# Optimization experiments

Measured on AMD Instinct MI355X. Metric: run time of the kernel, lower is better.

## Reference

```python
import jax, jax.numpy as jnp
import numpy as np

NUM_HEAD = 8   # in_channels // 64 for in_channels=512
DIM = 8        # per-head dim (== num_head in this module)
H_CH = NUM_HEAD * DIM  # 64
SCALE = DIM ** (-0.5)


def _conv(x, w, b, padding):
    # x: [N,C,H,W], w: [O,I,kh,kw]
    out = jax.lax.conv_general_dilated(
        x, w, window_strides=(1, 1), padding=padding,
        dimension_numbers=("NCHW", "OIHW", "NCHW"))
    return out + b[None, :, None, None]


def setup_inputs() -> dict:
    key = jax.random.key(0)
    ks = jax.random.split(key, 4)
    N, C, H, W = 4, 512, 48, 48
    x = jax.random.normal(ks[0], (N, C, H, W), dtype=jnp.float32)
    qkv_w = jax.random.normal(ks[1], (3 * H_CH, C, 1, 1), dtype=jnp.float32) * 0.05
    qkv_b = jnp.zeros((3 * H_CH,), dtype=jnp.float32)
    pos_w = jax.random.normal(ks[2], (H_CH, H_CH, 3, 3), dtype=jnp.float32) * 0.05
    pos_b = jnp.zeros((H_CH,), dtype=jnp.float32)
    res_w = jax.random.normal(ks[3], (C, H_CH, 1, 1), dtype=jnp.float32) * 0.05
    res_b = jnp.zeros((C,), dtype=jnp.float32)
    return {"x": x, "qkv_w": qkv_w, "qkv_b": qkv_b,
            "pos_w": pos_w, "pos_b": pos_b,
            "res_w": res_w, "res_b": res_b}


def reference(x, qkv_w, qkv_b, pos_w, pos_b, res_w, res_b):
    N, C, H, W = x.shape
    L = H * W
    # 1x1 conv QKV projection -> [N, 3h, H, W]
    qkv = _conv(x, qkv_w, qkv_b, "VALID")
    # [N, num_head, 3*dim, L]
    qkv = qkv.reshape(N, NUM_HEAD, 3 * DIM, L)
    q, k, v = qkv[:, :, :DIM], qkv[:, :, DIM:2 * DIM], qkv[:, :, 2 * DIM:]
    # attn = q^T @ k * scale : [N, nh, L, L], softmax over keys (last dim)
    attn = jnp.einsum("nhdq,nhdk->nhqk", q, k) * SCALE
    attn = jax.nn.softmax(attn, axis=-1)
    # out = v @ attn^T : [N, nh, dim, L]
    out = jnp.einsum("nhdk,nhqk->nhdq", v, attn)
    out = out.reshape(N, H_CH, H, W)
    # positional branch: 3x3 conv on v
    pos = _conv(v.reshape(N, H_CH, H, W), pos_w, pos_b, "SAME")
    out = out + pos
    # resume 1x1 conv -> [N, out_channels, H, W]
    return _conv(out, res_w, res_b, "VALID")
```

## Files before the change

### kernel.cpp

```cpp
#include <hip/hip_runtime.h>

#define L_ATT 2304
#define QSCALE_LOG2E 0.5100695712f

using bh8 = __attribute__((ext_vector_type(8))) short;
using f4  = __attribute__((ext_vector_type(4))) float;

#if __has_builtin(__builtin_amdgcn_exp2f)
#define EXP2(x) __builtin_amdgcn_exp2f(x)
#else
#define EXP2(x) exp2f(x)
#endif

__device__ inline short f2b(float f) {
    union { float f; unsigned u; } c; c.f = f;
    unsigned r = (c.u + 0x7FFFu + ((c.u >> 16) & 1u)) >> 16;
    return (short)r;
}
__device__ inline float b2f(short s) {
    union { unsigned u; float f; } c;
    c.u = ((unsigned)(unsigned short)s) << 16;
    return c.f;
}
__device__ inline int packhi(float lo, float hi) {
    return (int)__builtin_amdgcn_perm(__float_as_uint(hi), __float_as_uint(lo), 0x07060302u);
}

__global__ __launch_bounds__(256) void prep_kernel(
    const float* __restrict__ x, const float* __restrict__ qkv_w,
    const float* __restrict__ res_w, const float* __restrict__ pos_w,
    short* __restrict__ xt, short* __restrict__ wqb,
    short* __restrict__ reswb, short* __restrict__ wqp)
{
    __shared__ float s[64][68];
    const int g = blockIdx.x;
    if (g < 272) {
        int j = g * 256 + threadIdx.x;
        if (j < 24576) {
            float4 v = ((const float4*)qkv_w)[j];
            short4 o = { f2b(v.x), f2b(v.y), f2b(v.z), f2b(v.w) };
            *(short4*)(wqb + (size_t)j * 4) = o;
        } else if (j < 32768) {
            int idx = j - 24576;
            float4 v = ((const float4*)res_w)[idx];
            short4 o = { f2b(v.x), f2b(v.y), f2b(v.z), f2b(v.w) };
            *(short4*)(reswb + (size_t)idx * 4) = o;
        } else {
            int e = j - 32768;
            wqp[e] = f2b(pos_w[(size_t)(e & 4095) * 9 + (e >> 12)]);
        }
        return;
    }
    const int gg = g - 272;
    const int l0 = (gg % 36) * 64, k0 = ((gg / 36) & 7) * 64, n = gg / 288;
    const int tr = threadIdx.x >> 4, tc4 = (threadIdx.x & 15) * 4;
    const float* xp = x + ((size_t)n * 512 + k0) * L_ATT + l0;
#pragma unroll
    for (int r = 0; r < 4; ++r)
        *(float4*)&s[tr + r * 16][tc4] =
            *(const float4*)(xp + (size_t)(tr + r * 16) * L_ATT + tc4);
    __syncthreads();
    short* op = xt + ((size_t)n * L_ATT + l0) * 512 + k0;
#pragma unroll
    for (int r = 0; r < 4; ++r) {
        int l = tr + r * 16;
        short4 o = { f2b(s[tc4 + 0][l]), f2b(s[tc4 + 1][l]),
                     f2b(s[tc4 + 2][l]), f2b(s[tc4 + 3][l]) };
        *(short4*)(op + (size_t)l * 512 + tc4) = o;
    }
}

__global__ __launch_bounds__(256) void qkv_kernel(
    const short* __restrict__ xt, const short* __restrict__ wqb,
    const float* __restrict__ qkv_b, short* __restrict__ qt8,
    short* __restrict__ kt8, short* __restrict__ vt, short* __restrict__ vle)
{
    const int g = blockIdx.x;
    const int xcd = g & 7, rr = g >> 3;
    const int y = rr % 3, grp = rr / 3;
    const int code = grp * 8 + xcd;
    const int l0 = (code % 72) * 32, oc0 = y * 64, n = code / 72;

    const int lane = threadIdx.x & 63, wave = threadIdx.x >> 6;
    const int col = lane & 15, quad = lane >> 4;
    const int ocb = oc0 + wave * 16;

    f4 acc[2];
    acc[0] = (f4){0.f, 0.f, 0.f, 0.f};
    acc[1] = (f4){0.f, 0.f, 0.f, 0.f};

    const short* arow = wqb + (size_t)(ocb + col) * 512 + quad * 8;
    const short* brow = xt + ((size_t)n * L_ATT + l0 + col) * 512 + quad * 8;

#pragma unroll 4
    for (int k0 = 0; k0 < 512; k0 += 32) {
        bh8 af = *(const bh8*)(arow + k0);
        bh8 b0 = *(const bh8*)(brow + k0);
        bh8 b1 = *(const bh8*)(brow + (size_t)16 * 512 + k0);
        acc[0] = __builtin_amdgcn_mfma_f32_16x16x32_bf16(af, b0, acc[0], 0, 0, 0);
        acc[1] = __builtin_amdgcn_mfma_f32_16x16x32_bf16(af, b1, acc[1], 0, 0, 0);
    }

    const int obase = ocb + quad * 4;
    const int h = obase / 24;
    const int r0 = obase - h * 24;
    const int slice = n * 8 + h;

#pragma unroll
    for (int nt = 0; nt < 2; ++nt) {
        int l = l0 + nt * 16 + col;
        float v[4];
#pragma unroll
        for (int reg = 0; reg < 4; ++reg) v[reg] = acc[nt][reg] + qkv_b[obase + reg];
        if (r0 < 8) {
            short4 o = { f2b(v[0] * QSCALE_LOG2E), f2b(v[1] * QSCALE_LOG2E),
                         f2b(v[2] * QSCALE_LOG2E), f2b(v[3] * QSCALE_LOG2E) };
            *(short4*)(qt8 + ((size_t)slice * L_ATT + l) * 8 + r0) = o;
        } else if (r0 < 16) {
            short4 o = { f2b(v[0]), f2b(v[1]), f2b(v[2]), f2b(v[3]) };
            *(short4*)(kt8 + ((size_t)slice * L_ATT + l) * 8 + (r0 - 8)) = o;
        } else {
            short4 o = { f2b(v[0]), f2b(v[1]), f2b(v[2]), f2b(v[3]) };
            int d0 = r0 - 16;
#pragma unroll
            for (int reg = 0; reg < 4; ++reg)
                vt[((size_t)slice * 8 + d0 + reg) * L_ATT + l] = ((short*)&o)[reg];
            *(short4*)(vle + ((size_t)n * L_ATT + l) * 64 + h * 8 + d0) = o;
        }
    }
}

__global__ __launch_bounds__(256) void attnpos_kernel(
    const short* __restrict__ qt8, const short* __restrict__ kt8,
    const short* __restrict__ vt, const short* __restrict__ vle,
    const short* __restrict__ wqp, const float* __restrict__ pbias,
    float* __restrict__ pnum, float* __restrict__ pls, short* __restrict__ pcv)
{
    __shared__ short smem[2064];
    const int g = blockIdx.x;
    const int tid = threadIdx.x;
    const int lane = tid & 63, wave = tid >> 6;
    const int col = lane & 15, quad = lane >> 4;

    if (g < 1152) {
        const int h = g & 7, r = g >> 3;
        const int n = r / 36;
        const int rem = r - n * 36;
        const int qt = rem >> 1, half = rem & 1;
        const int q0 = qt * 128;
        const int kbase = half * 1152;
        const int slice = n * 8 + h;

        const short* qs  = qt8 + (size_t)slice * L_ATT * 8;
        const short* ks8 = kt8 + (size_t)slice * L_ATT * 8;
        const short* vb  = vt  + (size_t)slice * 8 * L_ATT;

        if (tid < 16) smem[2048 + tid] = (tid < 8) ? (short)0x3F80 : (short)0;

        bh8 zero8 = {0, 0, 0, 0, 0, 0, 0, 0};
        bh8 qf[2];
#pragma unroll
        for (int f = 0; f < 2; ++f) {
            qf[f] = zero8;
            if (quad == 0)
                qf[f] = *(const bh8*)(qs + (size_t)(q0 + wave * 32 + f * 16 + col) * 8);
        }

        const int kxor = (quad == 0) ? 512 : 0;
        int kidx[4];
#pragma unroll
        for (int nt = 0; nt < 4; ++nt)
            kidx[nt] = (quad == 0) ? (nt * 16 + col) * 8 : 2056;
        const int vxor = (col < 8) ? 512 : 0;
        int vidx[2];
#pragma unroll
        for (int ks = 0; ks < 2; ++ks)
            vidx[ks] = (col < 8)
                     ? 1024 + col * 64 + ((ks * 32 + quad * 8 + col * 8) & 63)
                     : ((col == 8) ? 2048 : 2056);

        const int ksl = ((lane >> 5) & 1) * 32 + ((lane >> 2) & 1) * 16
                      + ((lane >> 3) & 3) * 4 + (lane & 3);
        const int vd = lane >> 3, vkc = (lane & 7) * 8;
        const int vsl = 1024 + vd * 64 + ((vkc + vd * 8) & 63);

        if (wave == 0)
            *(uint4*)&smem[ksl * 8] = *(const uint4*)(ks8 + (size_t)(kbase + lane) * 8);
        else if (wave == 1)
            *(uint4*)&smem[vsl] = *(const uint4*)(vb + (size_t)vd * L_ATT + kbase + vkc);
        __syncthreads();

        f4 oacc[2];
        oacc[0] = (f4){0.f, 0.f, 0.f, 0.f};
        oacc[1] = (f4){0.f, 0.f, 0.f, 0.f};

        int sofs = 512;
        for (int t = 0; t < 18; ++t) {
            const int par = (t + 1) & 1;
            uint4 dk, dv;
            if (wave == par * 2)
                dk = *(const uint4*)(ks8 + (size_t)(kbase + (t + 1) * 64 + lane) * 8);
            else if (wave == par * 2 + 1)
                dv = *(const uint4*)(vb + (size_t)vd * L_ATT + kbase + (t + 1) * 64 + vkc);

            bh8 kf[4], vf[2];
#pragma unroll
            for (int nt = 0; nt < 4; ++nt) kf[nt] = *(const bh8*)&smem[kidx[nt]];
#pragma unroll
            for (int ks = 0; ks < 2; ++ks) vf[ks] = *(const bh8*)&smem[vidx[ks]];

            __builtin_amdgcn_s_setprio(1);
#pragma unroll
            for (int f = 0; f < 2; ++f) {
                f4 s[4];
#pragma unroll
                for (int nt = 0; nt < 4; ++nt) {
                    f4 z = (f4){0.f, 0.f, 0.f, 0.f};
                    s[nt] = __builtin_amdgcn_mfma_f32_16x16x32_bf16(kf[nt], qf[f], z, 0, 0, 0);
                }
                float e[4][4];
#pragma unroll
                for (int nt = 0; nt < 4; ++nt)
#pragma unroll
                    for (int reg = 0; reg < 4; ++reg)
                        e[nt][reg] = EXP2(s[nt][reg]);
#pragma unroll
                for (int ks = 0; ks < 2; ++ks) {
                    union { int i[4]; bh8 v; } pu;
                    pu.i[0] = packhi(e[2 * ks][0],     e[2 * ks][1]);
                    pu.i[1] = packhi(e[2 * ks][2],     e[2 * ks][3]);
                    pu.i[2] = packhi(e[2 * ks + 1][0], e[2 * ks + 1][1]);
                    pu.i[3] = packhi(e[2 * ks + 1][2], e[2 * ks + 1][3]);
                    oacc[f] = __builtin_amdgcn_mfma_f32_16x16x32_bf16(vf[ks], pu.v, oacc[f], 0, 0, 0);
                }
            }
            __builtin_amdgcn_s_setprio(0);

            if (wave == par * 2)          *(uint4*)&smem[sofs + ksl * 8] = dk;
            else if (wave == par * 2 + 1) *(uint4*)&smem[sofs + vsl] = dv;

#pragma unroll
            for (int nt = 0; nt < 4; ++nt) kidx[nt] ^= kxor;
            vidx[0] ^= vxor; vidx[1] ^= vxor;
            sofs ^= 512;
            __syncthreads();
        }

        const size_t prow = (size_t)(slice * 2 + half) * L_ATT;
#pragma unroll
        for (int f = 0; f < 2; ++f) {
            int qg = q0 + wave * 32 + f * 16 + col;
            if (quad < 2) {
                float4 o = { oacc[f][0], oacc[f][1], oacc[f][2], oacc[f][3] };
                *(float4*)(pnum + (prow + qg) * 8 + quad * 4) = o;
            } else if (quad == 2) {
                pls[prow + qg] = oacc[f][0];
            }
        }
        return;
    }

    const int gf = g - 1152;
    const int l0 = (gf % 144) * 16, n = gf / 144;
    const int t = wave;

    const int la = l0 + col;
    const int ya = la / 48, xa = la - ya * 48;

    f4 acc = (f4){0.f, 0.f, 0.f, 0.f};
    const short* vbase = vle + (size_t)n * L_ATT * 64;

#pragma unroll
    for (int q = 0; q < 9; ++q) {
        const int dy = q / 3 - 1, dx = q - (q / 3) * 3 - 1;
        const bool valid = ((unsigned)(ya + dy) < 48u) && ((unsigned)(xa + dx) < 48u);
        const short* ap = vbase + (size_t)(la + dy * 48 + dx) * 64 + quad * 8;
#pragma unroll
        for (int ks = 0; ks < 2; ++ks) {
            bh8 af = {0, 0, 0, 0, 0, 0, 0, 0};
            if (valid) af = *(const bh8*)(ap + ks * 32);
            bh8 bf = *(const bh8*)(wqp + ((size_t)q * 64 + t * 16 + col) * 64
                                   + ks * 32 + quad * 8);
            acc = __builtin_amdgcn_mfma_f32_16x16x32_bf16(af, bf, acc, 0, 0, 0);
        }
    }

    short* op = pcv + (size_t)n * L_ATT * 64;
    const int oc = t * 16 + col;
    const float bb = pbias[oc];
#pragma unroll
    for (int reg = 0; reg < 4; ++reg) {
        int l = l0 + quad * 4 + reg;
        op[(size_t)l * 64 + oc] = f2b(acc[reg] + bb);
    }
}

__global__ __launch_bounds__(256) void comb_kernel(
    const float* __restrict__ pnum, const float* __restrict__ pls,
    const short* __restrict__ pcv, short* __restrict__ battp)
{
    const int b = blockIdx.x;
    const int n = b / 144, lt = b % 144;
    const int hh = threadIdx.x & 15;
    const int l  = lt * 16 + (threadIdx.x >> 4);
    const int h = hh >> 1, dh = hh & 1;

    const size_t p0 = (size_t)((n * 8 + h) * 2) * L_ATT;
    const size_t p1 = p0 + L_ATT;
    float4 a = *(const float4*)(pnum + (p0 + l) * 8 + dh * 4);
    float4 c = *(const float4*)(pnum + (p1 + l) * 8 + dh * 4);
    float inv = 1.0f / (pls[p0 + l] + pls[p1 + l]);
    short4 pv = *(const short4*)(pcv + ((size_t)n * L_ATT + l) * 64 + hh * 4);

    int2 o;
    o.x = packhi((a.x + c.x) * inv + b2f(pv.x), (a.y + c.y) * inv + b2f(pv.y));
    o.y = packhi((a.z + c.z) * inv + b2f(pv.z), (a.w + c.w) * inv + b2f(pv.w));
    *(int2*)(battp + ((size_t)n * L_ATT + l) * 64 + hh * 4) = o;
}

__global__ __launch_bounds__(256) void res_kernel(
    const short* __restrict__ battp, const short* __restrict__ reswb,
    const float* __restrict__ res_b, float* __restrict__ out)
{
    const int g = blockIdx.x;
    const int xcd = g & 7, rr = g >> 3;
    const int y = rr & 7, grp = rr >> 3;
    const int code = grp * 8 + xcd;
    const int l0 = (code % 36) * 64, oc0 = y * 64, n = code / 36;

    const int lane = threadIdx.x & 63, wave = threadIdx.x >> 6;
    const int col = lane & 15, quad = lane >> 4;
    const int ocb = oc0 + wave * 16;

    f4 acc[4];
#pragma unroll
    for (int nt = 0; nt < 4; ++nt) acc[nt] = (f4){0.f, 0.f, 0.f, 0.f};

#pragma unroll
    for (int ks = 0; ks < 2; ++ks) {
        bh8 af = *(const bh8*)(reswb + (size_t)(ocb + col) * 64 + ks * 32 + quad * 8);
        const int ch = ks * 32 + quad * 8;
#pragma unroll
        for (int nt = 0; nt < 4; ++nt) {
            const int l = l0 + nt * 16 + col;
            bh8 bf = *(const bh8*)(battp + ((size_t)n * L_ATT + l) * 64 + ch);
            acc[nt] = __builtin_amdgcn_mfma_f32_16x16x32_bf16(af, bf, acc[nt], 0, 0, 0);
        }
    }

#pragma unroll
    for (int nt = 0; nt < 4; ++nt) {
        int l = l0 + nt * 16 + col;
#pragma unroll
        for (int reg = 0; reg < 4; ++reg) {
            int oc = ocb + quad * 4 + reg;
            out[((size_t)n * 512 + oc) * L_ATT + l] = acc[nt][reg] + res_b[oc];
        }
    }
}

extern "C" void kernel_launch(void* const* d_in, const int* in_sizes, int n_in,
                              void* d_out, int out_size, void* d_ws, size_t ws_size,
                              hipStream_t stream)
{
    const float* x      = (const float*)d_in[0];
    const float* qkv_w  = (const float*)d_in[1];
    const float* qkv_b  = (const float*)d_in[2];
    const float* pos_w  = (const float*)d_in[3];
    const float* pos_b  = (const float*)d_in[4];
    const float* res_w  = (const float*)d_in[5];
    const float* res_b  = (const float*)d_in[6];
    float* out = (float*)d_out;

    char* ws = (char*)d_ws;
    short* xt    = (short*)(ws);
    float* pnum  = (float*)(ws);
    float* pls   = (float*)(ws + 4718592);
    short* qt8   = (short*)(ws + 9437184);
    short* kt8   = (short*)(ws + 10616832);
    short* vt    = (short*)(ws + 11796480);
    short* pcv   = (short*)(ws + 12976128);
    short* wqb   = (short*)(ws + 14155776);
    short* reswb = (short*)(ws + 14352384);
    short* vle   = (short*)(ws + 14417920);
    short* wqp   = (short*)(ws + 15597568);
    short* battp = (short*)(ws + 15671296);

    prep_kernel<<<1424, 256, 0, stream>>>(x, qkv_w, res_w, pos_w, xt, wqb, reswb, wqp);
    qkv_kernel<<<864, 256, 0, stream>>>(xt, wqb, qkv_b, qt8, kt8, vt, vle);
    attnpos_kernel<<<1728, 256, 0, stream>>>(qt8, kt8, vt, vle, wqp, pos_b, pnum, pls, pcv);
    comb_kernel<<<576, 256, 0, stream>>>(pnum, pls, pcv, battp);
    res_kernel<<<1152, 256, 0, stream>>>(battp, reswb, res_b, out);
}
```

Measured before the change: 150.0 us.

## Stage two key/value tiles per iteration to halve barriers in attention loop

The attention loop now loads two 64-key K and V tiles per iteration instead of one. All four waves take part in the global prefetch: two fetch K and two fetch V, where previously only two waves loaded. The loop runs 9 iterations of two sub-tiles each, so the number of __syncthreads is halved. Shared memory roughly doubles to hold the double-buffered pairs, which may reduce how many blocks fit per CU.

New measurement: 148.8 us. No clear change (-0.8%).

```diff
diff --git a/kernel.cpp b/kernel.cpp
--- a/kernel.cpp
+++ b/kernel.cpp
@@ -136,7 +136,7 @@
     const short* __restrict__ wqp, const float* __restrict__ pbias,
     float* __restrict__ pnum, float* __restrict__ pls, short* __restrict__ pcv)
 {
-    __shared__ short smem[2064];
+    __shared__ short smem[4112];
     const int g = blockIdx.x;
     const int tid = threadIdx.x;
     const int lane = tid & 63, wave = tid >> 6;
@@ -155,7 +155,7 @@
         const short* ks8 = kt8 + (size_t)slice * L_ATT * 8;
         const short* vb  = vt  + (size_t)slice * 8 * L_ATT;
 
-        if (tid < 16) smem[2048 + tid] = (tid < 8) ? (short)0x3F80 : (short)0;
+        if (tid < 16) smem[4096 + tid] = (tid < 8) ? (short)0x3F80 : (short)0;
 
         bh8 zero8 = {0, 0, 0, 0, 0, 0, 0, 0};
         bh8 qf[2];
@@ -166,83 +166,86 @@
                 qf[f] = *(const bh8*)(qs + (size_t)(q0 + wave * 32 + f * 16 + col) * 8);
         }
 
-        const int kxor = (quad == 0) ? 512 : 0;
         int kidx[4];
 #pragma unroll
         for (int nt = 0; nt < 4; ++nt)
-            kidx[nt] = (quad == 0) ? (nt * 16 + col) * 8 : 2056;
-        const int vxor = (col < 8) ? 512 : 0;
+            kidx[nt] = (quad == 0) ? (nt * 16 + col) * 8 : 4104;
         int vidx[2];
 #pragma unroll
         for (int ks = 0; ks < 2; ++ks)
             vidx[ks] = (col < 8)
-                     ? 1024 + col * 64 + ((ks * 32 + quad * 8 + col * 8) & 63)
-                     : ((col == 8) ? 2048 : 2056);
+                     ? col * 64 + ((ks * 32 + quad * 8 + col * 8) & 63)
+                     : ((col == 8) ? 4096 : 4104);
 
         const int ksl = ((lane >> 5) & 1) * 32 + ((lane >> 2) & 1) * 16
                       + ((lane >> 3) & 3) * 4 + (lane & 3);
         const int vd = lane >> 3, vkc = (lane & 7) * 8;
-        const int vsl = 1024 + vd * 64 + ((vkc + vd * 8) & 63);
-
-        if (wave == 0)
-            *(uint4*)&smem[ksl * 8] = *(const uint4*)(ks8 + (size_t)(kbase + lane) * 8);
-        else if (wave == 1)
-            *(uint4*)&smem[vsl] = *(const uint4*)(vb + (size_t)vd * L_ATT + kbase + vkc);
+        const int vsl = vd * 64 + ((vkc + vd * 8) & 63);
+
+        if (wave < 2)
+            *(uint4*)&smem[wave * 512 + ksl * 8] =
+                *(const uint4*)(ks8 + (size_t)(kbase + wave * 64 + lane) * 8);
+        else
+            *(uint4*)&smem[2048 + (wave - 2) * 512 + vsl] =
+                *(const uint4*)(vb + (size_t)vd * L_ATT + kbase + (wave - 2) * 64 + vkc);
         __syncthreads();
 
         f4 oacc[2];
         oacc[0] = (f4){0.f, 0.f, 0.f, 0.f};
         oacc[1] = (f4){0.f, 0.f, 0.f, 0.f};
 
-        int sofs = 512;
-        for (int t = 0; t < 18; ++t) {
-            const int par = (t + 1) & 1;
-            uint4 dk, dv;
-            if (wave == par * 2)
-                dk = *(const uint4*)(ks8 + (size_t)(kbase + (t + 1) * 64 + lane) * 8);
-            else if (wave == par * 2 + 1)
-                dv = *(const uint4*)(vb + (size_t)vd * L_ATT + kbase + (t + 1) * 64 + vkc);
-
-            bh8 kf[4], vf[2];
-#pragma unroll
-            for (int nt = 0; nt < 4; ++nt) kf[nt] = *(const bh8*)&smem[kidx[nt]];
-#pragma unroll
-            for (int ks = 0; ks < 2; ++ks) vf[ks] = *(const bh8*)&smem[vidx[ks]];
-
-            __builtin_amdgcn_s_setprio(1);
-#pragma unroll
-            for (int f = 0; f < 2; ++f) {
-                f4 s[4];
-#pragma unroll
-                for (int nt = 0; nt < 4; ++nt) {
-                    f4 z = (f4){0.f, 0.f, 0.f, 0.f};
-                    s[nt] = __builtin_amdgcn_mfma_f32_16x16x32_bf16(kf[nt], qf[f], z, 0, 0, 0);
+        int p = 0;
+        for (int t = 0; t < 9; ++t) {
+            uint4 dst;
+            if (wave < 2)
+                dst = *(const uint4*)(ks8 + (size_t)(kbase + (t * 2 + 2 + wave) * 64 + lane) * 8);
+            else
+                dst = *(const uint4*)(vb + (size_t)vd * L_ATT
+                                      + kbase + (t * 2 + wave) * 64 + vkc);
+
+#pragma unroll
+            for (int u = 0; u < 2; ++u) {
+                const int ku = (quad == 0) ? p * 1024 + u * 512 : 0;
+                const int vu = (col < 8) ? 2048 + p * 1024 + u * 512 : 0;
+                bh8 kf[4], vf[2];
+#pragma unroll
+                for (int nt = 0; nt < 4; ++nt) kf[nt] = *(const bh8*)&smem[kidx[nt] + ku];
+#pragma unroll
+                for (int ks = 0; ks < 2; ++ks) vf[ks] = *(const bh8*)&smem[vidx[ks] + vu];
+
+                __builtin_amdgcn_s_setprio(1);
+#pragma unroll
+                for (int f = 0; f < 2; ++f) {
+                    f4 s[4];
+#pragma unroll
+                    for (int nt = 0; nt < 4; ++nt) {
+                        f4 z = (f4){0.f, 0.f, 0.f, 0.f};
+                        s[nt] = __builtin_amdgcn_mfma_f32_16x16x32_bf16(kf[nt], qf[f], z, 0, 0, 0);
+                    }
+                    float e[4][4];
+#pragma unroll
+                    for (int nt = 0; nt < 4; ++nt)
+#pragma unroll
+                        for (int reg = 0; reg < 4; ++reg)
+                            e[nt][reg] = EXP2(s[nt][reg]);
+#pragma unroll
+                    for (int ks = 0; ks < 2; ++ks) {
+                        union { int i[4]; bh8 v; } pu;
+                        pu.i[0] = packhi(e[2 * ks][0],     e[2 * ks][1]);
+                        pu.i[1] = packhi(e[2 * ks][2],     e[2 * ks][3]);
+                        pu.i[2] = packhi(e[2 * ks + 1][0], e[2 * ks + 1][1]);
+                        pu.i[3] = packhi(e[2 * ks + 1][2], e[2 * ks + 1][3]);
+                        oacc[f] = __builtin_amdgcn_mfma_f32_16x16x32_bf16(vf[ks], pu.v, oacc[f], 0, 0, 0);
+                    }
                 }
-                float e[4][4];
-#pragma unroll
-                for (int nt = 0; nt < 4; ++nt)
-#pragma unroll
-                    for (int reg = 0; reg < 4; ++reg)
-                        e[nt][reg] = EXP2(s[nt][reg]);
-#pragma unroll
-                for (int ks = 0; ks < 2; ++ks) {
-                    union { int i[4]; bh8 v; } pu;
-                    pu.i[0] = packhi(e[2 * ks][0],     e[2 * ks][1]);
-                    pu.i[1] = packhi(e[2 * ks][2],     e[2 * ks][3]);
-                    pu.i[2] = packhi(e[2 * ks + 1][0], e[2 * ks + 1][1]);
-                    pu.i[3] = packhi(e[2 * ks + 1][2], e[2 * ks + 1][3]);
-                    oacc[f] = __builtin_amdgcn_mfma_f32_16x16x32_bf16(vf[ks], pu.v, oacc[f], 0, 0, 0);
-                }
+                __builtin_amdgcn_s_setprio(0);
             }
-            __builtin_amdgcn_s_setprio(0);
-
-            if (wave == par * 2)          *(uint4*)&smem[sofs + ksl * 8] = dk;
-            else if (wave == par * 2 + 1) *(uint4*)&smem[sofs + vsl] = dv;
-
-#pragma unroll
-            for (int nt = 0; nt < 4; ++nt) kidx[nt] ^= kxor;
-            vidx[0] ^= vxor; vidx[1] ^= vxor;
-            sofs ^= 512;
+
+            if (wave < 2)
+                *(uint4*)&smem[(p ^ 1) * 1024 + wave * 512 + ksl * 8] = dst;
+            else
+                *(uint4*)&smem[2048 + (p ^ 1) * 1024 + (wave - 2) * 512 + vsl] = dst;
+            p ^= 1;
             __syncthreads();
         }
 
```
